# Optimization experiments

Hardware: AMD Instinct MI355X
Metric: run time of the kernel (lower is better)

The kernel has to match this reference:

```python
import jax, jax.numpy as jnp
import numpy as np

B, H, W, C, NH, WS, DEPTH = 32, 56, 56, 192, 6, 7, 2
SHIFTS = (0, WS // 2)
N = WS * WS
NW = (H // WS) * (W // WS)
HD = C // NH
SCALE = HD ** -0.5


def _rel_index():
    coords = np.stack(np.meshgrid(np.arange(WS), np.arange(WS), indexing='ij')).reshape(2, -1)
    rel = (coords[:, :, None] - coords[:, None, :]).transpose(1, 2, 0)
    rel[..., 0] += WS - 1
    rel[..., 1] += WS - 1
    rel[..., 0] *= 2 * WS - 1
    return jnp.asarray(rel.sum(-1))  # (N, N) int

REL_IDX = _rel_index()


def _attn_mask():
    # BasicLayer.creat_mask for the shifted block (shift = WS//2)
    img = np.zeros((H, W))
    sl = (slice(0, -WS), slice(-WS, -SHIFTS[1]), slice(-SHIFTS[1], None))
    cnt = 0
    for hs in sl:
        for ws_ in sl:
            img[hs, ws_] = cnt
            cnt += 1
    mw = img.reshape(H // WS, WS, W // WS, WS).transpose(0, 2, 1, 3).reshape(-1, N)
    d = mw[:, None, :] - mw[:, :, None]  # unsqueeze(1) - unsqueeze(2)
    return jnp.asarray(np.where(d != 0, -100.0, 0.0).astype(np.float32))  # (NW, N, N)

ATTN_MASK = _attn_mask()


def _ln(x, w, b):
    mu = x.mean(-1, keepdims=True)
    var = ((x - mu) ** 2).mean(-1, keepdims=True)
    return (x - mu) * jax.lax.rsqrt(var + 1e-5) * w + b


def _block(x, p, shift):
    Bn, L, Cc = x.shape
    shortcut = x
    h = _ln(x, p['n1w'], p['n1b']).reshape(Bn, H, W, Cc)
    if shift > 0:
        h = jnp.roll(h, (-shift, -shift), axis=(1, 2))
    # window_partition -> (Bn*NW, N, C)
    h = h.reshape(Bn, H // WS, WS, W // WS, WS, Cc).transpose(0, 1, 3, 2, 4, 5).reshape(-1, N, Cc)
    qkv = (h @ p['qkvw'].T + p['qkvb']).reshape(-1, N, 3, NH, HD).transpose(2, 0, 3, 1, 4)
    q, k, v = qkv[0] * SCALE, qkv[1], qkv[2]  # (Bw, NH, N, HD)
    attn = jnp.einsum('bhnd,bhmd->bhnm', q, k)
    bias = p['rpb'][REL_IDX].transpose(2, 0, 1)  # (NH, N, N)
    attn = attn + bias[None]
    if shift > 0:
        attn = attn.reshape(Bn, NW, NH, N, N) + ATTN_MASK[None, :, None]
        attn = attn.reshape(-1, NH, N, N)
    attn = jax.nn.softmax(attn, axis=-1)
    h = jnp.einsum('bhnm,bhmd->bhnd', attn, v).transpose(0, 2, 1, 3).reshape(-1, N, Cc)
    h = h @ p['projw'].T + p['projb']
    # window_reverse
    h = h.reshape(Bn, H // WS, W // WS, WS, WS, Cc).transpose(0, 1, 3, 2, 4, 5).reshape(Bn, H, W, Cc)
    if shift > 0:
        # NOTE: source rolls back by window_size (not shift_size); replicated faithfully
        h = jnp.roll(h, (WS, WS), axis=(1, 2))
    x = shortcut + h.reshape(Bn, L, Cc)
    m = _ln(x, p['n2w'], p['n2b'])
    m = jax.nn.gelu(m @ p['f1w'].T + p['f1b'], approximate=False) @ p['f2w'].T + p['f2b']
    return x + m


def setup_inputs() -> dict:
    key = jax.random.key(0)
    ks = jax.random.split(key, 15)
    r = lambda k, s, sc: jax.random.normal(k, s, dtype=jnp.float32) * sc
    return {
        'x': r(ks[0], (B, H * W, C), 1.0),
        'n1w': 1.0 + r(ks[1], (DEPTH, C), 0.01),
        'n1b': r(ks[2], (DEPTH, C), 0.01),
        'qkvw': r(ks[3], (DEPTH, 3 * C, C), 0.05),
        'qkvb': r(ks[4], (DEPTH, 3 * C), 0.01),
        'rpb': r(ks[5], (DEPTH, (2 * WS - 1) ** 2, NH), 0.02),
        'projw': r(ks[6], (DEPTH, C, C), 0.05),
        'projb': r(ks[7], (DEPTH, C), 0.01),
        'n2w': 1.0 + r(ks[8], (DEPTH, C), 0.01),
        'n2b': r(ks[9], (DEPTH, C), 0.01),
        'f1w': r(ks[10], (DEPTH, 4 * C, C), 0.05),
        'f1b': r(ks[11], (DEPTH, 4 * C), 0.01),
        'f2w': r(ks[12], (DEPTH, C, 4 * C), 0.05),
        'f2b': r(ks[13], (DEPTH, C), 0.01),
    }


def reference(x, n1w, n1b, qkvw, qkvb, rpb, projw, projb, n2w, n2b, f1w, f1b, f2w, f2b):
    for i in range(DEPTH):
        p = {'n1w': n1w[i], 'n1b': n1b[i], 'qkvw': qkvw[i], 'qkvb': qkvb[i],
             'rpb': rpb[i], 'projw': projw[i], 'projb': projb[i],
             'n2w': n2w[i], 'n2b': n2b[i], 'f1w': f1w[i], 'f1b': f1b[i],
             'f2w': f2w[i], 'f2b': f2b[i]}
        x = _block(x, p, SHIFTS[i])
    return x
```

## Files before the change

### kernel.cpp

```cpp
#include <hip/hip_runtime.h>
#include <hip/hip_bf16.h>
#include <math.h>

typedef __hip_bfloat16 bf16;

#define BB    32
#define HH    56
#define WWI   56
#define CC    192
#define NHH   6
#define WSS   7
#define NN    49
#define NWIN  64
#define HDD   32
#define LL    (HH*WWI)
#define ROWS  (BB*NWIN*NN)
#define TOT   ((size_t)ROWS*CC)
#define SCALEQ 0.17677669529663687f

#define OFF_N1W   0
#define OFF_N1B   384
#define OFF_QKVW  768
#define OFF_QKVB  221952
#define OFF_RPB   223104
#define OFF_PROJW 225132
#define OFF_PROJB 298860
#define OFF_N2W   299244
#define OFF_N2B   299628
#define OFF_F1W   300012
#define OFF_F1B   594924
#define OFF_F2W   596460
#define OFF_F2B   891372

typedef __bf16 bf16x8v __attribute__((ext_vector_type(8)));
typedef float  f32x4   __attribute__((ext_vector_type(4)));

__device__ __forceinline__ float tof(bf16 v){ return __bfloat162float(v); }
__device__ __forceinline__ bf16  tob(float v){ return __float2bfloat16(v); }
__device__ __forceinline__ float xload(const float* p){ return *p; }
__device__ __forceinline__ float xload(const bf16*  p){ return tof(*p); }
__device__ __forceinline__ void  xstore(float* p, float v){ *p = v; }
__device__ __forceinline__ void  xstore(bf16*  p, float v){ *p = tob(v); }

__device__ __forceinline__ bf16x8v ldfrag(const bf16* p){
    return *(const bf16x8v*)p;
}
__device__ __forceinline__ unsigned short bfbits(float v){
    bf16 b = tob(v);
    return __builtin_bit_cast(unsigned short, b);
}
__device__ __forceinline__ bf16 mkbf(unsigned short u){
    return __builtin_bit_cast(bf16, u);
}

template<typename XT>
__device__ __forceinline__ float ldx(const void* p, size_t i, int dynf){
    if (dynf < 0) return xload(((const XT*)p) + i);
    return dynf ? tof(((const bf16*)p)[i]) : ((const float*)p)[i];
}

__device__ __forceinline__ float fast_gelu(float x){
    float u = fabsf(x) * 0.70710678118f;
    float t = __builtin_amdgcn_rcpf(1.f + 0.3275911f*u);
    float p = t*(0.254829592f + t*(-0.284496736f + t*(1.421413741f +
              t*(-1.453152027f + t*1.061405429f))));
    float e = __expf(-u*u);
    float erfu = 1.f - p*e;
    float s = copysignf(erfu, x);
    return 0.5f*x*(1.f + s);
}

__global__ void k_detect(const unsigned short* __restrict__ w, int* __restrict__ flag){
    if (blockIdx.x == 0 && threadIdx.x == 0){
        int cnt = 0;
        for (int k = 0; k < 16; ++k){
            unsigned short u = w[2*k];
            if (u >= 0x3E00 && u <= 0x4100) ++cnt;
        }
        *flag = (cnt >= 8) ? 1 : 0;
    }
}

__global__ void k_canon(const void* __restrict__ src, bf16* __restrict__ dst,
                        int n, const int* __restrict__ flag){
    int i = blockIdx.x * blockDim.x + threadIdx.x;
    if (i >= n) return;
    if (*flag) dst[i] = ((const bf16*)src)[i];
    else       dst[i] = tob(((const float*)src)[i]);
}

template<typename XT>
__global__ __launch_bounds__(256) void k_out(const XT* __restrict__ X,
        void* __restrict__ out, const int* __restrict__ flag){
    size_t i = ((size_t)blockIdx.x * 256 + threadIdx.x) * 8;
    if (i >= TOT) return;
    float v[8];
    if constexpr (sizeof(XT) == 4){
        f32x4 a = *(const f32x4*)((const float*)X + i);
        f32x4 b = *(const f32x4*)((const float*)X + i + 4);
        #pragma unroll
        for (int e = 0; e < 4; ++e){ v[e] = a[e]; v[4+e] = b[e]; }
    } else {
        bf16x8v a = ldfrag((const bf16*)X + i);
        #pragma unroll
        for (int e = 0; e < 8; ++e) v[e] = tof(mkbf(__builtin_bit_cast(unsigned short, a[e])));
    }
    if (*flag){
        bf16x8v o;
        #pragma unroll
        for (int e = 0; e < 8; ++e) o[e] = __builtin_bit_cast(__bf16, bfbits(v[e]));
        *(bf16x8v*)((bf16*)out + i) = o;
    } else {
        f32x4 o0, o1;
        #pragma unroll
        for (int e = 0; e < 4; ++e){ o0[e] = v[e]; o1[e] = v[4+e]; }
        *(f32x4*)((float*)out + i)     = o0;
        *(f32x4*)((float*)out + i + 4) = o1;
    }
}

template<typename XT>
__global__ __launch_bounds__(256) void k_ln_part(const void* __restrict__ src,
        int dynsrc, const int* __restrict__ flag,
        const bf16* __restrict__ w, const bf16* __restrict__ bsh,
        bf16* __restrict__ Hwin, int shift){
    int dynf = dynsrc ? flag[0] : -1;
    int wv = threadIdx.x >> 6, lane = threadIdx.x & 63;
    int row = blockIdx.x*4 + wv;
    int b   = row / (NWIN*NN);
    int win = (row / NN) % NWIN;
    int n   = row % NN;
    int wh = win >> 3, ww = win & 7;
    int iy = n / WSS, ix = n % WSS;
    int sy = (wh*WSS + iy + shift) % HH;
    int sx = (ww*WSS + ix + shift) % WWI;
    size_t base = ((size_t)(b*LL + sy*WWI + sx))*CC;
    float v0 = ldx<XT>(src, base + lane,       dynf);
    float v1 = ldx<XT>(src, base + lane + 64,  dynf);
    float v2 = ldx<XT>(src, base + lane + 128, dynf);
    float sm  = v0+v1+v2;
    float sm2 = v0*v0+v1*v1+v2*v2;
    #pragma unroll
    for (int st = 1; st < 64; st <<= 1){
        sm  += __shfl_xor(sm,  st);
        sm2 += __shfl_xor(sm2, st);
    }
    float mu  = sm * (1.f/CC);
    float inv = rsqrtf(sm2*(1.f/CC) - mu*mu + 1e-5f);
    bf16* dst = Hwin + (size_t)row*CC;
    dst[lane]     = tob((v0-mu)*inv*tof(w[lane])     + tof(bsh[lane]));
    dst[lane+64]  = tob((v1-mu)*inv*tof(w[lane+64])  + tof(bsh[lane+64]));
    dst[lane+128] = tob((v2-mu)*inv*tof(w[lane+128]) + tof(bsh[lane+128]));
}

__device__ __forceinline__ int mt0(int i){ return (i < 3) ? i*16 : 33; }

#define OL_ST 200
template<typename XT>
__global__ __launch_bounds__(512, 4) void k_attn(const bf16* __restrict__ Hwin,
        const bf16* __restrict__ qkvw, const bf16* __restrict__ qkvb,
        const bf16* __restrict__ rpb,
        const bf16* __restrict__ pw, const bf16* __restrict__ pb,
        const void* rsrc, int dynsrc, const int* __restrict__ flag,
        XT* __restrict__ X, int masked){
    __shared__ bf16 smem[31104];
    bf16* qls = smem;
    bf16* kls = smem + 9408;
    bf16* vT  = smem + 18816;
    bf16* Pls = smem;
    bf16* OLs = smem;

    int fl = dynsrc ? flag[0] : 0;
    int t = threadIdx.x;
    int win  = blockIdx.x;
    int winl = win & (NWIN-1);
    int wh = winl >> 3, ww = winl & 7;
    int wv = t >> 6, lane = t & 63;
    int li16 = lane & 15, quad = lane >> 4;

    for (int idx = t; idx < 192*15; idx += 512){
        int d = idx / 15, tokp = 49 + idx % 15;
        vT[d*64 + (tokp ^ ((d&7)<<3))] = tob(0.f);
    }

    {
        int p = wv & 1, c = wv >> 1;
        int m0a = mt0(2*p), m0b = mt0(2*p+1);
        const bf16* hg = Hwin + (size_t)win*NN*CC;
        bf16x8v afa[6], afb[6];
        #pragma unroll
        for (int kc = 0; kc < 6; ++kc){
            afa[kc] = ldfrag(hg + (m0a+li16)*CC + kc*32 + quad*8);
            afb[kc] = ldfrag(hg + (m0b+li16)*CC + kc*32 + quad*8);
        }
        #pragma unroll 3
        for (int j = 0; j < 9; ++j){
            int nt = c + 4*j;
            int col = nt*16 + li16;
            f32x4 acc0 = {0.f,0.f,0.f,0.f}, acc1 = {0.f,0.f,0.f,0.f};
            #pragma unroll
            for (int kc = 0; kc < 6; ++kc){
                bf16x8v bfr = ldfrag(qkvw + (size_t)col*CC + kc*32 + quad*8);
                acc0 = __builtin_amdgcn_mfma_f32_16x16x32_bf16(afa[kc], bfr, acc0, 0, 0, 0);
                acc1 = __builtin_amdgcn_mfma_f32_16x16x32_bf16(afb[kc], bfr, acc1, 0, 0, 0);
            }
            float bias = tof(qkvb[col]);
            int m  = col / CC;
            int cm = col - m*CC;
            #pragma unroll
            for (int r = 0; r < 4; ++r){
                int rowA = m0a + quad*4 + r;
                int rowB = m0b + quad*4 + r;
                float v0 = acc0[r] + bias, v1 = acc1[r] + bias;
                if (m == 0){
                    qls[rowA*CC + (cm ^ ((rowA&7)<<3))] = tob(v0*SCALEQ);
                    qls[rowB*CC + (cm ^ ((rowB&7)<<3))] = tob(v1*SCALEQ);
                } else if (m == 1){
                    kls[rowA*CC + (cm ^ ((rowA&7)<<3))] = tob(v0);
                    kls[rowB*CC + (cm ^ ((rowB&7)<<3))] = tob(v1);
                } else {
                    vT[cm*64 + (rowA ^ ((cm&7)<<3))] = tob(v0);
                    vT[cm*64 + (rowB ^ ((cm&7)<<3))] = tob(v1);
                }
            }
        }
    }
    __syncthreads();

    unsigned int pk[3][8];
    #pragma unroll
    for (int j = 0; j < 3; ++j){
        int id = wv + 8*j;
        int mt = id & 3, h = id >> 2;
        int m0 = mt0(mt);
        int rowq = m0 + li16;
        bf16x8v afr = ldfrag(qls + rowq*CC + ((h*32 + quad*8) ^ ((rowq&7)<<3)));
        f32x4 s[4];
        #pragma unroll
        for (int nt = 0; nt < 4; ++nt){
            int rowk = nt*16 + li16;
            bf16x8v bfr = ldfrag(kls + rowk*CC + ((h*32 + quad*8) ^ ((rowk&7)<<3)));
            f32x4 z = {0.f,0.f,0.f,0.f};
            s[nt] = __builtin_amdgcn_mfma_f32_16x16x32_bf16(afr, bfr, z, 0, 0, 0);
        }
        #pragma unroll
        for (int nt = 0; nt < 4; ++nt){
            int jj = nt*16 + li16;
            int valid = (jj < NN);
            int jc = valid ? jj : 48;
            int yj = (jc*37) >> 8, xj = jc - 7*yj;
            int lj = 0;
            if (masked){
                int ayj = wh*WSS + yj, axj = ww*WSS + xj;
                lj = ((ayj<49)?0:(ayj<53)?1:2)*3 + ((axj<49)?0:(axj<53)?1:2);
            }
            #pragma unroll
            for (int r = 0; r < 4; ++r){
                int i = m0 + quad*4 + r;
                int yi = (i*37) >> 8, xi = i - 7*yi;
                int ridx = (yi - yj + 6)*13 + (xi - xj + 6);
                float v = s[nt][r] + tof(rpb[ridx*NHH + h]);
                if (masked){
                    int ayi = wh*WSS + yi, axi = ww*WSS + xi;
                    int li = ((ayi<49)?0:(ayi<53)?1:2)*3 + ((axi<49)?0:(axi<53)?1:2);
                    if (li != lj) v -= 100.f;
                }
                s[nt][r] = valid ? v : -1e30f;
            }
        }
        float mx[4], sm[4];
        #pragma unroll
        for (int r = 0; r < 4; ++r)
            mx[r] = fmaxf(fmaxf(s[0][r], s[1][r]), fmaxf(s[2][r], s[3][r]));
        #pragma unroll
        for (int st = 1; st < 16; st <<= 1){
            #pragma unroll
            for (int r = 0; r < 4; ++r) mx[r] = fmaxf(mx[r], __shfl_xor(mx[r], st));
        }
        #pragma unroll
        for (int nt = 0; nt < 4; ++nt){
            #pragma unroll
            for (int r = 0; r < 4; ++r) s[nt][r] = __expf(s[nt][r] - mx[r]);
        }
        #pragma unroll
        for (int r = 0; r < 4; ++r) sm[r] = (s[0][r]+s[1][r]) + (s[2][r]+s[3][r]);
        #pragma unroll
        for (int st = 1; st < 16; st <<= 1){
            #pragma unroll
            for (int r = 0; r < 4; ++r) sm[r] += __shfl_xor(sm[r], st);
        }
        #pragma unroll
        for (int r = 0; r < 4; ++r) sm[r] = 1.f / sm[r];
        #pragma unroll
        for (int nt = 0; nt < 4; ++nt){
            #pragma unroll
            for (int rr = 0; rr < 2; ++rr){
                unsigned int u0 = bfbits(s[nt][2*rr]   * sm[2*rr]);
                unsigned int u1 = bfbits(s[nt][2*rr+1] * sm[2*rr+1]);
                pk[j][nt*2+rr] = (u1 << 16) | u0;
            }
        }
    }
    __syncthreads();

    #pragma unroll
    for (int j = 0; j < 3; ++j){
        int id = wv + 8*j;
        int m0 = mt0(id & 3), h = id >> 2;
        #pragma unroll
        for (int nt = 0; nt < 4; ++nt){
            int jj = nt*16 + li16;
            #pragma unroll
            for (int rr = 0; rr < 2; ++rr){
                unsigned int u = pk[j][nt*2+rr];
                int tok0 = m0 + quad*4 + 2*rr;
                int tok1 = tok0 + 1;
                Pls[(h*NN + tok0)*64 + (jj ^ ((tok0&7)<<3))] = mkbf((unsigned short)(u & 0xffff));
                Pls[(h*NN + tok1)*64 + (jj ^ ((tok1&7)<<3))] = mkbf((unsigned short)(u >> 16));
            }
        }
    }
    __syncthreads();

    f32x4 oacc[6];
    {
        int mt = wv & 3, nto = wv >> 2;
        int m0 = mt0(mt), n0 = nto*16;
        #pragma unroll
        for (int h = 0; h < NHH; ++h){
            f32x4 acc = {0.f,0.f,0.f,0.f};
            #pragma unroll
            for (int kc = 0; kc < 2; ++kc){
                int rowp = m0 + li16;
                bf16x8v afr = ldfrag(Pls + (h*NN + rowp)*64 + ((kc*32 + quad*8) ^ ((rowp&7)<<3)));
                int rowv = h*HDD + n0 + li16;
                bf16x8v bfr = ldfrag(vT + rowv*64 + ((kc*32 + quad*8) ^ ((rowv&7)<<3)));
                acc = __builtin_amdgcn_mfma_f32_16x16x32_bf16(afr, bfr, acc, 0, 0, 0);
            }
            oacc[h] = acc;
        }
    }
    __syncthreads();

    {
        int mt = wv & 3, nto = wv >> 2;
        int m0 = mt0(mt), n0 = nto*16;
        #pragma unroll
        for (int h = 0; h < NHH; ++h){
            #pragma unroll
            for (int r = 0; r < 4; ++r){
                int tok = m0 + quad*4 + r;
                OLs[tok*OL_ST + h*HDD + n0 + li16] = tob(oacc[h][r]);
            }
        }
    }
    __syncthreads();

    {
        int b = win >> 6;
        int roll = masked ? WSS : 0;
        int mthalf = wv >> 2, ntg = wv & 3;
        #pragma unroll
        for (int j = 0; j < 3; ++j){
            int col = (ntg*3 + j)*16 + li16;
            bf16x8v bfr[6];
            #pragma unroll
            for (int kc = 0; kc < 6; ++kc)
                bfr[kc] = ldfrag(pw + (size_t)col*CC + kc*32 + quad*8);
            float bias = tof(pb[col]);
            #pragma unroll
            for (int mtl = 0; mtl < 2; ++mtl){
                int m0 = mt0(mthalf*2 + mtl);
                f32x4 acc = {0.f,0.f,0.f,0.f};
                #pragma unroll
                for (int kc = 0; kc < 6; ++kc){
                    bf16x8v afr = ldfrag(OLs + (m0 + li16)*OL_ST + kc*32 + quad*8);
                    acc = __builtin_amdgcn_mfma_f32_16x16x32_bf16(afr, bfr[kc], acc, 0, 0, 0);
                }
                #pragma unroll
                for (int r = 0; r < 4; ++r){
                    int tok = m0 + quad*4 + r;
                    if (m0 == 33 && tok != 48) continue;
                    int iy = (tok*37) >> 8, ix = tok - 7*iy;
                    int y = (wh*WSS + iy + roll) % HH;
                    int x = (ww*WSS + ix + roll) % WWI;
                    size_t idx = ((size_t)(b*LL + y*WWI + x))*CC + col;
                    float res;
                    if (dynsrc)
                        res = fl ? tof(((const bf16*)rsrc)[idx])
                                 : ((const float*)rsrc)[idx];
                    else
                        res = xload(&X[idx]);
                    xstore(&X[idx], res + acc[r] + bias);
                }
            }
        }
    }
}

template<typename XT>
__global__ __launch_bounds__(256, 3) void k_mlp(XT* __restrict__ X,
        const bf16* __restrict__ n2w, const bf16* __restrict__ n2b,
        const bf16* __restrict__ w1, const bf16* __restrict__ b1,
        const bf16* __restrict__ w2, const bf16* __restrict__ b2){
    __shared__ bf16 xin[64*192];
    __shared__ bf16 h1p[64*192];
    int t = threadIdx.x;
    int wv = t >> 6, lane = t & 63;
    int li16 = lane & 15, quad = lane >> 4;
    size_t row0 = (size_t)blockIdx.x * 64;

    {
        float nw0 = tof(n2w[lane]), nw1 = tof(n2w[lane+64]), nw2 = tof(n2w[lane+128]);
        float nb0 = tof(n2b[lane]), nb1 = tof(n2b[lane+64]), nb2 = tof(n2b[lane+128]);
        #pragma unroll 4
        for (int i = 0; i < 16; ++i){
            int r = wv*16 + i;
            const XT* xr = X + (row0 + r)*CC;
            float v0 = xload(&xr[lane]);
            float v1 = xload(&xr[lane+64]);
            float v2 = xload(&xr[lane+128]);
            float sm  = v0+v1+v2;
            float sm2 = v0*v0+v1*v1+v2*v2;
            #pragma unroll
            for (int st = 1; st < 64; st <<= 1){
                sm  += __shfl_xor(sm,  st);
                sm2 += __shfl_xor(sm2, st);
            }
            float mu  = sm * (1.f/CC);
            float inv = rsqrtf(sm2*(1.f/CC) - mu*mu + 1e-5f);
            int swz = (r&7)<<3;
            bf16* xrow = xin + r*192;
            xrow[lane        ^ swz] = tob((v0-mu)*inv*nw0 + nb0);
            xrow[(lane+64)   ^ swz] = tob((v1-mu)*inv*nw1 + nb1);
            xrow[(lane+128)  ^ swz] = tob((v2-mu)*inv*nw2 + nb2);
        }
    }
    __syncthreads();

    int sw = (li16 & 7) << 3;
    f32x4 acc2[3][4];
    #pragma unroll
    for (int j = 0; j < 3; ++j)
        #pragma unroll
        for (int m = 0; m < 4; ++m)
            acc2[j][m] = (f32x4){0.f,0.f,0.f,0.f};

    #pragma unroll 1
    for (int pass = 0; pass < 4; ++pass){
        #pragma unroll
        for (int j = 0; j < 3; ++j){
            int cl  = (wv*3 + j)*16 + li16;
            int col = pass*192 + cl;
            f32x4 a1[4];
            #pragma unroll
            for (int m = 0; m < 4; ++m) a1[m] = (f32x4){0.f,0.f,0.f,0.f};
            #pragma unroll
            for (int kc = 0; kc < 6; ++kc){
                bf16x8v bfr = ldfrag(w1 + (size_t)col*CC + kc*32 + quad*8);
                #pragma unroll
                for (int m = 0; m < 4; ++m){
                    bf16x8v af = ldfrag(xin + (m*16 + li16)*192 + ((kc*32 + quad*8) ^ sw));
                    a1[m] = __builtin_amdgcn_mfma_f32_16x16x32_bf16(af, bfr, a1[m], 0, 0, 0);
                }
            }
            float bb = tof(b1[col]);
            #pragma unroll
            for (int m = 0; m < 4; ++m){
                #pragma unroll
                for (int r = 0; r < 4; ++r){
                    int row = m*16 + quad*4 + r;
                    h1p[row*192 + (cl ^ ((row&7)<<3))] = tob(fast_gelu(a1[m][r] + bb));
                }
            }
        }
        __syncthreads();
        #pragma unroll
        for (int kc = 0; kc < 6; ++kc){
            bf16x8v af[4];
            #pragma unroll
            for (int m = 0; m < 4; ++m)
                af[m] = ldfrag(h1p + (m*16 + li16)*192 + ((kc*32 + quad*8) ^ sw));
            int kg = pass*6 + kc;
            #pragma unroll
            for (int j = 0; j < 3; ++j){
                int col = wv*48 + j*16 + li16;
                bf16x8v bfr = ldfrag(w2 + (size_t)col*768 + kg*32 + quad*8);
                #pragma unroll
                for (int m = 0; m < 4; ++m)
                    acc2[j][m] = __builtin_amdgcn_mfma_f32_16x16x32_bf16(af[m], bfr, acc2[j][m], 0, 0, 0);
            }
        }
        __syncthreads();
    }

    #pragma unroll
    for (int j = 0; j < 3; ++j){
        int col = wv*48 + j*16 + li16;
        float bias = tof(b2[col]);
        #pragma unroll
        for (int m = 0; m < 4; ++m){
            #pragma unroll
            for (int r = 0; r < 4; ++r){
                size_t idx = (row0 + m*16 + quad*4 + r)*CC + col;
                xstore(&X[idx], xload(&X[idx]) + acc2[j][m][r] + bias);
            }
        }
    }
}

template<typename XT>
static void run_pipeline(const bf16* wb, const void* xin0, int* flag,
                         XT* X, bf16* Hwin, void* out,
                         hipStream_t stream){
    for (int i = 0; i < 2; ++i){
        int shift = i ? (WSS/2) : 0;
        const void* src = (i == 0) ? xin0 : (const void*)X;
        int dynsrc = (i == 0) ? 1 : 0;
        k_ln_part<XT><<<ROWS/4, 256, 0, stream>>>(src, dynsrc, flag,
                wb+OFF_N1W + i*CC, wb+OFF_N1B + i*CC, Hwin, shift);
        k_attn<XT><<<BB*NWIN, 512, 0, stream>>>(Hwin,
                wb+OFF_QKVW + (size_t)i*3*CC*CC, wb+OFF_QKVB + (size_t)i*3*CC,
                wb+OFF_RPB + (size_t)i*169*NHH,
                wb+OFF_PROJW + (size_t)i*CC*CC, wb+OFF_PROJB + i*CC,
                src, dynsrc, flag, X, i);
        k_mlp<XT><<<ROWS/64, 256, 0, stream>>>(X,
                wb+OFF_N2W + i*CC, wb+OFF_N2B + i*CC,
                wb+OFF_F1W + (size_t)i*4*CC*CC, wb+OFF_F1B + (size_t)i*4*CC,
                wb+OFF_F2W + (size_t)i*CC*4*CC, wb+OFF_F2B + i*CC);
    }
    k_out<XT><<<(int)(TOT/2048), 256, 0, stream>>>(X, out, flag);
}

extern "C" void kernel_launch(void* const* d_in, const int* in_sizes, int n_in,
                              void* d_out, int out_size, void* d_ws, size_t ws_size,
                              hipStream_t stream){
    char* p = (char*)d_ws;
    int*  flag = (int*)p;
    bf16* wb   = (bf16*)(p + 16);
    char* q    = p + 16 + (2u<<20);

    k_detect<<<1, 64, 0, stream>>>((const unsigned short*)d_in[1], flag);

    static const int widx[13] = {1,2,3,4,5,6,7,8,9,10,11,12,13};
    static const int woff[13] = {OFF_N1W,OFF_N1B,OFF_QKVW,OFF_QKVB,OFF_RPB,
                                 OFF_PROJW,OFF_PROJB,OFF_N2W,OFF_N2B,
                                 OFF_F1W,OFF_F1B,OFF_F2W,OFF_F2B};
    static const int wsz[13]  = {384,384,221184,1152,2028,73728,384,384,384,
                                 294912,1536,294912,384};
    for (int k = 0; k < 13; ++k)
        k_canon<<<(wsz[k]+255)/256, 256, 0, stream>>>(d_in[widx[k]], wb+woff[k],
                                                      wsz[k], flag);

    size_t needF32 = 16 + (2u<<20) + TOT*4 + TOT*2;
    if (ws_size >= needF32){
        float* X   = (float*)q;       q += TOT*4;
        bf16* Hwin = (bf16*)q;
        run_pipeline<float>(wb, d_in[0], flag, X, Hwin, d_out, stream);
    } else {
        bf16* X    = (bf16*)q;        q += TOT*2;
        bf16* Hwin = (bf16*)q;
        run_pipeline<bf16>(wb, d_in[0], flag, X, Hwin, d_out, stream);
    }
}
```

Measured before the change: 1.090 ms.

## Stage projection output in LDS for coalesced residual writes; cache rel-pos bias in LDS

The projection GEMM results, with bias added, are now written to shared memory. A separate pass then does the residual read-modify-write in 8-element contiguous chunks per token, replacing scattered per-lane column stores. The relative position bias table is also copied into LDS so the attention-score loop reads it locally instead of from global memory. This costs about 2 KB more LDS, an extra barrier, and rounding the projection output to bf16 before the residual add.

```diff
diff --git a/kernel.cpp b/kernel.cpp
--- a/kernel.cpp
+++ b/kernel.cpp
@@ -162,13 +162,15 @@
         const bf16* __restrict__ rpb,
         const bf16* __restrict__ pw, const bf16* __restrict__ pb,
         const void* rsrc, int dynsrc, const int* __restrict__ flag,
-        XT* __restrict__ X, int masked){
-    __shared__ bf16 smem[31104];
-    bf16* qls = smem;
-    bf16* kls = smem + 9408;
-    bf16* vT  = smem + 18816;
-    bf16* Pls = smem;
-    bf16* OLs = smem;
+        XT* X, int masked){
+    __shared__ bf16 smem[32128];
+    bf16* qls  = smem;
+    bf16* kls  = smem + 9408;
+    bf16* vT   = smem + 18816;
+    bf16* rpbl = smem + 31104;
+    bf16* Pls  = smem;
+    bf16* OLs  = smem;
+    bf16* projout = smem + 18816;
 
     int fl = dynsrc ? flag[0] : 0;
     int t = threadIdx.x;
@@ -182,6 +184,7 @@
         int d = idx / 15, tokp = 49 + idx % 15;
         vT[d*64 + (tokp ^ ((d&7)<<3))] = tob(0.f);
     }
+    for (int idx = t; idx < 169*NHH; idx += 512) rpbl[idx] = rpb[idx];
 
     {
         int p = wv & 1, c = wv >> 1;
@@ -259,7 +262,7 @@
                 int i = m0 + quad*4 + r;
                 int yi = (i*37) >> 8, xi = i - 7*yi;
                 int ridx = (yi - yj + 6)*13 + (xi - xj + 6);
-                float v = s[nt][r] + tof(rpb[ridx*NHH + h]);
+                float v = s[nt][r] + tof(rpbl[ridx*NHH + h]);
                 if (masked){
                     int ayi = wh*WSS + yi, axi = ww*WSS + xi;
                     int li = ((ayi<49)?0:(ayi<53)?1:2)*3 + ((axi<49)?0:(axi<53)?1:2);
@@ -357,8 +360,6 @@
     __syncthreads();
 
     {
-        int b = win >> 6;
-        int roll = masked ? WSS : 0;
         int mthalf = wv >> 2, ntg = wv & 3;
         #pragma unroll
         for (int j = 0; j < 3; ++j){
@@ -380,18 +381,43 @@
                 #pragma unroll
                 for (int r = 0; r < 4; ++r){
                     int tok = m0 + quad*4 + r;
-                    if (m0 == 33 && tok != 48) continue;
-                    int iy = (tok*37) >> 8, ix = tok - 7*iy;
-                    int y = (wh*WSS + iy + roll) % HH;
-                    int x = (ww*WSS + ix + roll) % WWI;
-                    size_t idx = ((size_t)(b*LL + y*WWI + x))*CC + col;
-                    float res;
-                    if (dynsrc)
-                        res = fl ? tof(((const bf16*)rsrc)[idx])
-                                 : ((const float*)rsrc)[idx];
-                    else
-                        res = xload(&X[idx]);
-                    xstore(&X[idx], res + acc[r] + bias);
+                    projout[tok*192 + col] = tob(acc[r] + bias);
+                }
+            }
+        }
+    }
+    __syncthreads();
+
+    {
+        int b = win >> 6;
+        int roll = masked ? WSS : 0;
+        for (int c = t; c < NN*24; c += 512){
+            int tok = c / 24, c8 = c % 24;
+            int iy = tok / WSS, ix = tok % WSS;
+            int y = (wh*WSS + iy + roll) % HH;
+            int x = (ww*WSS + ix + roll) % WWI;
+            size_t idx = ((size_t)(b*LL + y*WWI + x))*CC + c8*8;
+            float pv[8];
+            #pragma unroll
+            for (int e = 0; e < 8; ++e) pv[e] = tof(projout[tok*192 + c8*8 + e]);
+            if (dynsrc){
+                float v[8];
+                if (fl){
+                    const bf16* rp = (const bf16*)rsrc;
+                    #pragma unroll
+                    for (int e = 0; e < 8; ++e) v[e] = tof(rp[idx + e]);
+                } else {
+                    const float* rp = (const float*)rsrc;
+                    #pragma unroll
+                    for (int e = 0; e < 8; ++e) v[e] = rp[idx + e];
+                }
+                #pragma unroll
+                for (int e = 0; e < 8; ++e) xstore(&X[idx + e], v[e] + pv[e]);
+            } else {
+                #pragma unroll
+                for (int e = 0; e < 8; ++e){
+                    float v = xload(&X[idx + e]) + pv[e];
+                    xstore(&X[idx + e], v);
                 }
             }
         }
```

New measurement: 970.0 us. -11.0%, faster.
